# Optimization experiments

Hardware: AMD Instinct MI355X
Metric: run time of the kernel (lower is better)

Reference implementation:

```python
import jax, jax.numpy as jnp
import numpy as np


def setup_inputs() -> dict:
    key = jax.random.key(0)
    k1, k2 = jax.random.split(key)
    q, k, d5 = 128, 2048, 768
    return {
        "tgt": jax.random.normal(k1, (q, d5), dtype=jnp.float32),
        "memory": jax.random.normal(k2, (k, d5), dtype=jnp.float32),
        "seq_len": 32,
    }


def reference(tgt, memory, seq_len):
    q, d5 = tgt.shape
    k, _ = memory.shape
    z = d5 // seq_len  # per-token sub-dim
    query_t = tgt.reshape(q, seq_len, z)    # [q, t, d]
    key_m = memory.reshape(k, seq_len, z)   # [k, s, d]
    # Full late-interaction similarity tensor [q, k, s, t]
    score = jnp.einsum('qtd,ksd->qkst', query_t, key_m)
    # max over memory tokens (s) and over query tokens (t), concat, mean
    pooled = jnp.concatenate((score.max(axis=2), score.max(axis=3)), axis=-1)  # [q, k, 2*seq_len]
    score_p = jax.nn.sigmoid(pooled.mean(axis=-1))  # [q, k]
    return (score_p, score_p)
```

## Files before the change

kernel.cpp:

```cpp
#include <hip/hip_runtime.h>
#include <hip/hip_bf16.h>

typedef __bf16 bf16x8 __attribute__((ext_vector_type(8)));
typedef short  s16x4  __attribute__((ext_vector_type(4)));
typedef float  f32x16 __attribute__((ext_vector_type(16)));
typedef int    i32x2  __attribute__((ext_vector_type(2)));

constexpr int QN  = 128;
constexpr int KN  = 2048;
constexpr int D5  = 768;
constexpr int SL  = 32;
constexpr int ZD  = 24;
constexpr int KCH = 16;
constexpr int WPB = 8;

#if __has_builtin(__builtin_amdgcn_mfma_f32_32x32x8bf16_1k)
#define HAVE_MFMA_X8 1
#else
#define HAVE_MFMA_X8 0
#endif

#if __has_builtin(__builtin_amdgcn_permlane32_swap)
#define HAVE_PERMLANE32 1
#else
#define HAVE_PERMLANE32 0
#endif

static __device__ __forceinline__ float max3f(float a, float b, float c) {
    return fmaxf(fmaxf(a, b), c);
}

static __device__ __forceinline__ float redmax16(const f32x16& a) {
    float x0 = max3f(a[0],  a[1],  a[2]);
    float x1 = max3f(a[3],  a[4],  a[5]);
    float x2 = max3f(a[6],  a[7],  a[8]);
    float x3 = max3f(a[9],  a[10], a[11]);
    float x4 = max3f(a[12], a[13], a[14]);
    float y0 = max3f(x0, x1, x2);
    float y1 = max3f(x3, x4, a[15]);
    return fmaxf(y0, y1);
}

static __device__ __forceinline__ float halfmax(float m) {
#if HAVE_PERMLANE32
    i32x2 pr = __builtin_amdgcn_permlane32_swap(__builtin_bit_cast(int, m),
                                                __builtin_bit_cast(int, m),
                                                false, false);
    return fmaxf(__builtin_bit_cast(float, pr[0]), __builtin_bit_cast(float, pr[1]));
#else
    return fmaxf(m, __shfl_xor(m, 32));
#endif
}

#if HAVE_MFMA_X8
static __device__ __forceinline__ short f2bfbits(float x) {
    __bf16 b = (__bf16)x;
    return __builtin_bit_cast(short, b);
}
#endif

__global__ __launch_bounds__(512, 8) void matcher_kernel(const float* __restrict__ tgt,
                                                         const float* __restrict__ mem,
                                                         float* __restrict__ out)
{
    __shared__ __align__(16) __bf16 Kf[KCH * 768];
    __shared__ float vbuf[WPB][KCH * 32];

    const int tid = threadIdx.x;
    const int qg  = blockIdx.x;
    const int kc  = blockIdx.y;
    const int k0  = kc * KCH;

    {
        const int r  = tid;
        const int kl = r >> 5;
        const int s  = r & 31;
        const float* src = mem + (size_t)(k0 + kl) * D5 + s * ZD;
        float tv[24];
#pragma unroll
        for (int j = 0; j < 6; ++j) ((float4*)tv)[j] = ((const float4*)src)[j];
        bf16x8 a, b, c;
#pragma unroll
        for (int j = 0; j < 8; ++j) {
            a[j] = (__bf16)tv[j];
            b[j] = (__bf16)tv[8 + j];
            c[j] = (__bf16)tv[16 + j];
        }
        __bf16* base = Kf + kl * 768;
        *(bf16x8*)(base +        s * 8)  = a;
        *(bf16x8*)(base + (32 +  s) * 8) = b;
        *(bf16x8*)(base + 512 +  s * 8)  = c;
    }

    const int lane = tid & 63;
    const int wv   = tid >> 6;
    const int t    = lane & 31;
    const int h    = lane >> 5;
    const int q    = qg * WPB + wv;

    const float4* p4 = (const float4*)(tgt + (size_t)q * D5 + t * ZD);
    bf16x8 aQ0;
    {
        float4 u0 = p4[2 * h], u1 = p4[2 * h + 1];
        aQ0[0] = (__bf16)u0.x; aQ0[1] = (__bf16)u0.y; aQ0[2] = (__bf16)u0.z; aQ0[3] = (__bf16)u0.w;
        aQ0[4] = (__bf16)u1.x; aQ0[5] = (__bf16)u1.y; aQ0[6] = (__bf16)u1.z; aQ0[7] = (__bf16)u1.w;
    }
#if HAVE_MFMA_X8
    s16x4 aQ1;
    {
        float4 w = p4[4 + h];
        aQ1[0] = f2bfbits(w.x); aQ1[1] = f2bfbits(w.y);
        aQ1[2] = f2bfbits(w.z); aQ1[3] = f2bfbits(w.w);
    }
#else
    bf16x8 aQ1;
    if (h == 0) {
        float4 w0 = p4[4], w1 = p4[5];
        aQ1[0] = (__bf16)w0.x; aQ1[1] = (__bf16)w0.y; aQ1[2] = (__bf16)w0.z; aQ1[3] = (__bf16)w0.w;
        aQ1[4] = (__bf16)w1.x; aQ1[5] = (__bf16)w1.y; aQ1[6] = (__bf16)w1.z; aQ1[7] = (__bf16)w1.w;
    } else {
#pragma unroll
        for (int j = 0; j < 8; ++j) aQ1[j] = (__bf16)0.0f;
    }
#endif

    f32x16 zacc;
#pragma unroll
    for (int i = 0; i < 16; ++i) zacc[i] = 0.0f;

    __syncthreads();

    float* vb = vbuf[wv];

#pragma unroll 4
    for (int kl = 0; kl < KCH; ++kl) {
        const __bf16* lb = Kf + kl * 768;
        bf16x8 bK0 = *(const bf16x8*)(lb + lane * 8);
#if HAVE_MFMA_X8
        s16x4 bK1 = *(const s16x4*)(lb + 512 + t * 8 + h * 4);

        f32x16 accS = __builtin_amdgcn_mfma_f32_32x32x16_bf16(aQ0, bK0, zacc, 0, 0, 0);
        accS = __builtin_amdgcn_mfma_f32_32x32x8bf16_1k(aQ1, bK1, accS, 0, 0, 0);
        f32x16 accT = __builtin_amdgcn_mfma_f32_32x32x16_bf16(bK0, aQ0, zacc, 0, 0, 0);
        accT = __builtin_amdgcn_mfma_f32_32x32x8bf16_1k(bK1, aQ1, accT, 0, 0, 0);
#else
        bf16x8 bK1 = *(const bf16x8*)(lb + 512 + t * 8);

        f32x16 accS = __builtin_amdgcn_mfma_f32_32x32x16_bf16(aQ0, bK0, zacc, 0, 0, 0);
        accS        = __builtin_amdgcn_mfma_f32_32x32x16_bf16(aQ1, bK1, accS, 0, 0, 0);
        f32x16 accT = __builtin_amdgcn_mfma_f32_32x32x16_bf16(bK0, aQ0, zacc, 0, 0, 0);
        accT        = __builtin_amdgcn_mfma_f32_32x32x16_bf16(bK1, aQ1, accT, 0, 0, 0);
#endif
        float m1 = halfmax(redmax16(accS));
        float m2 = halfmax(redmax16(accT));
        float v = m1 + m2;
        if (h == 0) vb[(kl << 5) + (t ^ kl)] = v;
    }

    {
        const int p    = lane & 15;
        const int half = (lane >> 4) & 1;
        float x[16];
#pragma unroll
        for (int i = 0; i < 16; ++i)
            x[i] = vb[(p << 5) + ((half << 4) + i ^ p)];
        float s0 = (x[0] + x[1]) + (x[2] + x[3]);
        float s1 = (x[4] + x[5]) + (x[6] + x[7]);
        float s2 = (x[8] + x[9]) + (x[10] + x[11]);
        float s3 = (x[12] + x[13]) + (x[14] + x[15]);
        float sum = (s0 + s1) + (s2 + s3);
        sum += __shfl_xor(sum, 16);
        float r = 1.0f / (1.0f + __expf(-sum * (1.0f / 64.0f)));
        if (lane < 16) {
            const int idx = q * KN + k0 + p;
            out[idx] = r;
            out[idx + QN * KN] = r;
        }
    }
}

extern "C" void kernel_launch(void* const* d_in, const int* in_sizes, int n_in,
                              void* d_out, int out_size, void* d_ws, size_t ws_size,
                              hipStream_t stream)
{
    const float* tgt = (const float*)d_in[0];
    const float* mem = (const float*)d_in[1];
    float* out = (float*)d_out;
    dim3 grid(QN / WPB, KN / KCH);
    matcher_kernel<<<grid, 512, 0, stream>>>(tgt, mem, out);
}
```

Measured before the change: 89.64 us.

## Process multiple K chunks per block with register-prefetched double-buffered LDS

```diff
diff --git a/kernel.cpp b/kernel.cpp
--- a/kernel.cpp
+++ b/kernel.cpp
@@ -2,6 +2,7 @@
 #include <hip/hip_bf16.h>
 
 typedef __bf16 bf16x8 __attribute__((ext_vector_type(8)));
+typedef __bf16 bf16x4 __attribute__((ext_vector_type(4)));
 typedef short  s16x4  __attribute__((ext_vector_type(4)));
 typedef float  f32x16 __attribute__((ext_vector_type(16)));
 typedef int    i32x2  __attribute__((ext_vector_type(2)));
@@ -11,8 +12,9 @@
 constexpr int D5  = 768;
 constexpr int SL  = 32;
 constexpr int ZD  = 24;
-constexpr int KCH = 16;
+constexpr int KCH = 8;
 constexpr int WPB = 8;
+constexpr int NKC = 4;
 
 #if __has_builtin(__builtin_amdgcn_mfma_f32_32x32x8bf16_1k)
 #define HAVE_MFMA_X8 1
@@ -63,33 +65,26 @@
                                                          const float* __restrict__ mem,
                                                          float* __restrict__ out)
 {
-    __shared__ __align__(16) __bf16 Kf[KCH * 768];
+    __shared__ __align__(16) __bf16 Kf[2][KCH * 768];
     __shared__ float vbuf[WPB][KCH * 32];
 
     const int tid = threadIdx.x;
     const int qg  = blockIdx.x;
-    const int kc  = blockIdx.y;
-    const int k0  = kc * KCH;
-
-    {
-        const int r  = tid;
-        const int kl = r >> 5;
-        const int s  = r & 31;
-        const float* src = mem + (size_t)(k0 + kl) * D5 + s * ZD;
-        float tv[24];
-#pragma unroll
-        for (int j = 0; j < 6; ++j) ((float4*)tv)[j] = ((const float4*)src)[j];
-        bf16x8 a, b, c;
-#pragma unroll
-        for (int j = 0; j < 8; ++j) {
-            a[j] = (__bf16)tv[j];
-            b[j] = (__bf16)tv[8 + j];
-            c[j] = (__bf16)tv[16 + j];
-        }
-        __bf16* base = Kf + kl * 768;
-        *(bf16x8*)(base +        s * 8)  = a;
-        *(bf16x8*)(base + (32 +  s) * 8) = b;
-        *(bf16x8*)(base + 512 +  s * 8)  = c;
+    const int kcg = blockIdx.y;
+
+    const int sr  = tid & 255;
+    const int hf  = tid >> 8;
+    const int skl = sr >> 5;
+    const int ss  = sr & 31;
+
+    float4 pf0, pf1, pf2;
+
+    {
+        const int k0c = (kcg * NKC + 0) * KCH;
+        const float* src = mem + (size_t)(k0c + skl) * D5 + ss * ZD + hf * 12;
+        pf0 = ((const float4*)src)[0];
+        pf1 = ((const float4*)src)[1];
+        pf2 = ((const float4*)src)[2];
     }
 
     const int lane = tid & 63;
@@ -128,53 +123,109 @@
 #pragma unroll
     for (int i = 0; i < 16; ++i) zacc[i] = 0.0f;
 
+    {
+        __bf16* base = Kf[0] + skl * 768;
+        if (hf == 0) {
+            bf16x8 a;
+            a[0] = (__bf16)pf0.x; a[1] = (__bf16)pf0.y; a[2] = (__bf16)pf0.z; a[3] = (__bf16)pf0.w;
+            a[4] = (__bf16)pf1.x; a[5] = (__bf16)pf1.y; a[6] = (__bf16)pf1.z; a[7] = (__bf16)pf1.w;
+            *(bf16x8*)(base + ss * 8) = a;
+            bf16x4 b;
+            b[0] = (__bf16)pf2.x; b[1] = (__bf16)pf2.y; b[2] = (__bf16)pf2.z; b[3] = (__bf16)pf2.w;
+            *(bf16x4*)(base + (32 + ss) * 8) = b;
+        } else {
+            bf16x4 b;
+            b[0] = (__bf16)pf0.x; b[1] = (__bf16)pf0.y; b[2] = (__bf16)pf0.z; b[3] = (__bf16)pf0.w;
+            *(bf16x4*)(base + (32 + ss) * 8 + 4) = b;
+            bf16x8 cdat;
+            cdat[0] = (__bf16)pf1.x; cdat[1] = (__bf16)pf1.y; cdat[2] = (__bf16)pf1.z; cdat[3] = (__bf16)pf1.w;
+            cdat[4] = (__bf16)pf2.x; cdat[5] = (__bf16)pf2.y; cdat[6] = (__bf16)pf2.z; cdat[7] = (__bf16)pf2.w;
+            *(bf16x8*)(base + 512 + ss * 8) = cdat;
+        }
+    }
     __syncthreads();
 
     float* vb = vbuf[wv];
 
+    for (int c = 0; c < NKC; ++c) {
+        const int buf = c & 1;
+        const int k0  = (kcg * NKC + c) * KCH;
+
+        if (c + 1 < NKC) {
+            const int k0n = k0 + KCH;
+            const float* src = mem + (size_t)(k0n + skl) * D5 + ss * ZD + hf * 12;
+            pf0 = ((const float4*)src)[0];
+            pf1 = ((const float4*)src)[1];
+            pf2 = ((const float4*)src)[2];
+        }
+
 #pragma unroll 4
-    for (int kl = 0; kl < KCH; ++kl) {
-        const __bf16* lb = Kf + kl * 768;
-        bf16x8 bK0 = *(const bf16x8*)(lb + lane * 8);
+        for (int kl = 0; kl < KCH; ++kl) {
+            const __bf16* lb = Kf[buf] + kl * 768;
+            bf16x8 bK0 = *(const bf16x8*)(lb + lane * 8);
 #if HAVE_MFMA_X8
-        s16x4 bK1 = *(const s16x4*)(lb + 512 + t * 8 + h * 4);
-
-        f32x16 accS = __builtin_amdgcn_mfma_f32_32x32x16_bf16(aQ0, bK0, zacc, 0, 0, 0);
-        accS = __builtin_amdgcn_mfma_f32_32x32x8bf16_1k(aQ1, bK1, accS, 0, 0, 0);
-        f32x16 accT = __builtin_amdgcn_mfma_f32_32x32x16_bf16(bK0, aQ0, zacc, 0, 0, 0);
-        accT = __builtin_amdgcn_mfma_f32_32x32x8bf16_1k(bK1, aQ1, accT, 0, 0, 0);
-#else
-        bf16x8 bK1 = *(const bf16x8*)(lb + 512 + t * 8);
-
-        f32x16 accS = __builtin_amdgcn_mfma_f32_32x32x16_bf16(aQ0, bK0, zacc, 0, 0, 0);
-        accS        = __builtin_amdgcn_mfma_f32_32x32x16_bf16(aQ1, bK1, accS, 0, 0, 0);
-        f32x16 accT = __builtin_amdgcn_mfma_f32_32x32x16_bf16(bK0, aQ0, zacc, 0, 0, 0);
-        accT        = __builtin_amdgcn_mfma_f32_32x32x16_bf16(bK1, aQ1, accT, 0, 0, 0);
-#endif
-        float m1 = halfmax(redmax16(accS));
-        float m2 = halfmax(redmax16(accT));
-        float v = m1 + m2;
-        if (h == 0) vb[(kl << 5) + (t ^ kl)] = v;
-    }
-
-    {
-        const int p    = lane & 15;
-        const int half = (lane >> 4) & 1;
-        float x[16];
+            s16x4 bK1 = *(const s16x4*)(lb + 512 + t * 8 + h * 4);
+
+            f32x16 accS = __builtin_amdgcn_mfma_f32_32x32x16_bf16(aQ0, bK0, zacc, 0, 0, 0);
+            accS = __builtin_amdgcn_mfma_f32_32x32x8bf16_1k(aQ1, bK1, accS, 0, 0, 0);
+            f32x16 accT = __builtin_amdgcn_mfma_f32_32x32x16_bf16(bK0, aQ0, zacc, 0, 0, 0);
+            accT = __builtin_amdgcn_mfma_f32_32x32x8bf16_1k(bK1, aQ1, accT, 0, 0, 0);
+#else
+            bf16x8 bK1 = *(const bf16x8*)(lb + 512 + t * 8);
+
+            f32x16 accS = __builtin_amdgcn_mfma_f32_32x32x16_bf16(aQ0, bK0, zacc, 0, 0, 0);
+            accS        = __builtin_amdgcn_mfma_f32_32x32x16_bf16(aQ1, bK1, accS, 0, 0, 0);
+            f32x16 accT = __builtin_amdgcn_mfma_f32_32x32x16_bf16(bK0, aQ0, zacc, 0, 0, 0);
+            accT        = __builtin_amdgcn_mfma_f32_32x32x16_bf16(bK1, aQ1, accT, 0, 0, 0);
+#endif
+            float m1 = halfmax(redmax16(accS));
+            float m2 = halfmax(redmax16(accT));
+            float v = m1 + m2;
+            if (h == 0) vb[(kl << 5) + (t ^ kl)] = v;
+        }
+
+        {
+            const int p    = lane & 7;
+            const int half = (lane >> 3) & 1;
+            float x[16];
 #pragma unroll
-        for (int i = 0; i < 16; ++i)
-            x[i] = vb[(p << 5) + ((half << 4) + i ^ p)];
-        float s0 = (x[0] + x[1]) + (x[2] + x[3]);
-        float s1 = (x[4] + x[5]) + (x[6] + x[7]);
-        float s2 = (x[8] + x[9]) + (x[10] + x[11]);
-        float s3 = (x[12] + x[13]) + (x[14] + x[15]);
-        float sum = (s0 + s1) + (s2 + s3);
-        sum += __shfl_xor(sum, 16);
-        float r = 1.0f / (1.0f + __expf(-sum * (1.0f / 64.0f)));
-        if (lane < 16) {
-            const int idx = q * KN + k0 + p;
-            out[idx] = r;
-            out[idx + QN * KN] = r;
+            for (int i = 0; i < 16; ++i)
+                x[i] = vb[(p << 5) + (((half << 4) + i) ^ p)];
+            float s0 = (x[0] + x[1]) + (x[2] + x[3]);
+            float s1 = (x[4] + x[5]) + (x[6] + x[7]);
+            float s2 = (x[8] + x[9]) + (x[10] + x[11]);
+            float s3 = (x[12] + x[13]) + (x[14] + x[15]);
+            float sum = (s0 + s1) + (s2 + s3);
+            sum += __shfl_xor(sum, 8);
+            float r = 1.0f / (1.0f + __expf(-sum * (1.0f / 64.0f)));
+            if (lane < 8) {
+                const int idx = q * KN + k0 + p;
+                out[idx] = r;
+                out[idx + QN * KN] = r;
+            }
+        }
+
+        if (c + 1 < NKC) {
+            __syncthreads();
+            __bf16* base = Kf[buf ^ 1] + skl * 768;
+            if (hf == 0) {
+                bf16x8 a;
+                a[0] = (__bf16)pf0.x; a[1] = (__bf16)pf0.y; a[2] = (__bf16)pf0.z; a[3] = (__bf16)pf0.w;
+                a[4] = (__bf16)pf1.x; a[5] = (__bf16)pf1.y; a[6] = (__bf16)pf1.z; a[7] = (__bf16)pf1.w;
+                *(bf16x8*)(base + ss * 8) = a;
+                bf16x4 b;
+                b[0] = (__bf16)pf2.x; b[1] = (__bf16)pf2.y; b[2] = (__bf16)pf2.z; b[3] = (__bf16)pf2.w;
+                *(bf16x4*)(base + (32 + ss) * 8) = b;
+            } else {
+                bf16x4 b;
+                b[0] = (__bf16)pf0.x; b[1] = (__bf16)pf0.y; b[2] = (__bf16)pf0.z; b[3] = (__bf16)pf0.w;
+                *(bf16x4*)(base + (32 + ss) * 8 + 4) = b;
+                bf16x8 cdat;
+                cdat[0] = (__bf16)pf1.x; cdat[1] = (__bf16)pf1.y; cdat[2] = (__bf16)pf1.z; cdat[3] = (__bf16)pf1.w;
+                cdat[4] = (__bf16)pf2.x; cdat[5] = (__bf16)pf2.y; cdat[6] = (__bf16)pf2.z; cdat[7] = (__bf16)pf2.w;
+                *(bf16x8*)(base + 512 + ss * 8) = cdat;
+            }
+            __syncthreads();
         }
     }
 }
@@ -186,6 +237,6 @@
     const float* tgt = (const float*)d_in[0];
     const float* mem = (const float*)d_in[1];
     float* out = (float*)d_out;
-    dim3 grid(QN / WPB, KN / KCH);
+    dim3 grid(QN / WPB, KN / (KCH * NKC));
     matcher_kernel<<<grid, 512, 0, stream>>>(tgt, mem, out);
 }
```

Result: slower. 101.1 us (+12.8%).
